# Kernel optimization log

Measured on AMD Instinct MI355X. Metric: run time of the kernel, lower is better.

## Reference

```python
import jax, jax.numpy as jnp
import numpy as np

N = 8192       # number of points
C = 16         # num_colors (size of color distribution)
DIM = 2        # spatial dim (GeometricLoss(dim=2))


def setup_inputs() -> dict:
    key = jax.random.key(0)
    k1, k2 = jax.random.split(key)
    outputs = jax.random.normal(k1, (N, C), dtype=jnp.float32)
    points = jax.random.normal(k2, (N, DIM), dtype=jnp.float32)
    return {"outputs": outputs, "points": points, "k": 5}


def reference(outputs, points, k):
    # cdist(points, points) via the squared-norm expansion (avoids [N,N,dim] tensor)
    sq = jnp.sum(points * points, axis=1)                      # [N]
    d2 = sq[:, None] + sq[None, :] - 2.0 * (points @ points.T)  # [N,N]
    dist = jnp.sqrt(jnp.maximum(d2, 0.0))
    # k+1 smallest distances per row; drop self (distance 0)
    _, idx = jax.lax.top_k(-dist, k + 1)                        # [N,k+1]
    idx = idx[:, 1:]                                            # [N,k]
    neighbor_outputs = outputs[idx]                             # [N,k,C] gather
    # ||out_i - out_j|| over color dim, mean over all (i, neighbor) pairs
    differences = jnp.linalg.norm(outputs[:, None, :] - neighbor_outputs, axis=2)
    return differences.mean()
```

## Files before the change

### kernel.cpp

```cpp
#include <hip/hip_runtime.h>


static constexpr int NPTS    = 8192;
static constexpr int KNN     = 5;
static constexpr int CH      = 16;
static constexpr int QPB     = 4;
static constexpr int THREADS = 256;
static constexpr int NBLK    = NPTS / QPB;
static constexpr int CAP     = 128;
static constexpr int NF4     = NPTS / 2;
static constexpr int ITERS   = NF4 / THREADS;
static constexpr int BAT     = 4;
static constexpr int NB      = ITERS / BAT;

__device__ __forceinline__ unsigned long long shfl_xor_u64(unsigned long long v, int m) {
    unsigned int lo = (unsigned int)v;
    unsigned int hi = (unsigned int)(v >> 32);
    lo = __shfl_xor(lo, m, 64);
    hi = __shfl_xor(hi, m, 64);
    return ((unsigned long long)hi << 32) | lo;
}

__global__ __launch_bounds__(256, 8) void knn_loss_kernel(
        const float* __restrict__ outputs,
        const float* __restrict__ points,
        float* __restrict__ partial) {
    const int tid  = threadIdx.x;
    const int wave = tid >> 6;
    const int lane = tid & 63;
    const int qbase = blockIdx.x * QPB;

    const float2* __restrict__ pts2 = (const float2*)points;
    const float4* __restrict__ pts4 = (const float4*)points;
    const float FINF = __int_as_float(0x7f800000);

    float pix[QPB], piy[QPB];
    #pragma unroll
    for (int q = 0; q < QPB; ++q) {
        const float2 p = pts2[qbase + q];
        pix[q] = p.x; piy[q] = p.y;
    }

    float acc[QPB];
    #pragma unroll
    for (int q = 0; q < QPB; ++q) acc[q] = FINF;

    for (int b = 0; b < NB; ++b) {
        float4 p[BAT];
        #pragma unroll
        for (int u = 0; u < BAT; ++u)
            p[u] = pts4[b * (BAT * THREADS) + u * THREADS + tid];
        #pragma unroll
        for (int u = 0; u < BAT; ++u) {
            #pragma unroll
            for (int q = 0; q < QPB; ++q) {
                const float dxa = pix[q] - p[u].x, dya = piy[q] - p[u].y;
                const float dxb = pix[q] - p[u].z, dyb = piy[q] - p[u].w;
                const float d2a = fmaf(dxa, dxa, dya * dya);
                const float d2b = fmaf(dxb, dxb, dyb * dyb);
                acc[q] = fminf(fminf(acc[q], d2a), d2b);
            }
        }
    }

    __shared__ float thrmin[QPB][THREADS];
    __shared__ unsigned long long buf[QPB][CAP];
    __shared__ int cnt[QPB];
    __shared__ float Ts[QPB];
    __shared__ float red[QPB];

    #pragma unroll
    for (int q = 0; q < QPB; ++q)
        thrmin[q][tid] = fmaxf(acc[q], 0.0f);
    if (tid < QPB) cnt[tid] = 0;
    __syncthreads();

    {
        const float4 tv = ((const float4*)thrmin[wave])[lane];
        float v = fminf(fminf(tv.x, tv.y), fminf(tv.z, tv.w));
        float T = 0.0f;
        #pragma unroll
        for (int t = 0; t < KNN + 1; ++t) {
            float m = v;
            #pragma unroll
            for (int d = 1; d < 64; d <<= 1) m = fminf(m, __shfl_xor(m, d, 64));
            if (v == m) v = FINF;
            T = m;
        }
        if (lane == 0) Ts[wave] = T;
    }
    __syncthreads();

    float Tq[QPB];
    #pragma unroll
    for (int q = 0; q < QPB; ++q) Tq[q] = Ts[q];

    for (int b = 0; b < NB; ++b) {
        float4 p[BAT];
        #pragma unroll
        for (int u = 0; u < BAT; ++u)
            p[u] = pts4[b * (BAT * THREADS) + u * THREADS + tid];
        #pragma unroll
        for (int u = 0; u < BAT; ++u) {
            const int it = b * (BAT * THREADS) + u * THREADS + tid;
            float g = FINF;
            #pragma unroll
            for (int q = 0; q < QPB; ++q) {
                const float dxa = pix[q] - p[u].x, dya = piy[q] - p[u].y;
                const float dxb = pix[q] - p[u].z, dyb = piy[q] - p[u].w;
                const float d2a = fmaf(dxa, dxa, dya * dya);
                const float d2b = fmaf(dxb, dxb, dyb * dyb);
                g = fminf(g, fminf(d2a, d2b) - Tq[q]);
            }
            if (g <= 0.0f) {
                #pragma unroll
                for (int q = 0; q < QPB; ++q) {
                    const float dxa = pix[q] - p[u].x, dya = piy[q] - p[u].y;
                    const float dxb = pix[q] - p[u].z, dyb = piy[q] - p[u].w;
                    const float d2a = fmaf(dxa, dxa, dya * dya);
                    const float d2b = fmaf(dxb, dxb, dyb * dyb);
                    if (d2a <= Tq[q]) {
                        const int pos = atomicAdd(&cnt[q], 1);
                        if (pos < CAP)
                            buf[q][pos] =
                                ((unsigned long long)__float_as_uint(fmaxf(d2a, 0.0f)) << 32)
                                | (unsigned int)(2 * it);
                    }
                    if (d2b <= Tq[q]) {
                        const int pos = atomicAdd(&cnt[q], 1);
                        if (pos < CAP)
                            buf[q][pos] =
                                ((unsigned long long)__float_as_uint(fmaxf(d2b, 0.0f)) << 32)
                                | (unsigned int)(2 * it + 1);
                    }
                }
            }
        }
    }
    __syncthreads();

    const unsigned long long INF64 = ~0ull;
    const int n = min(cnt[wave], CAP);
    unsigned long long a  = (lane      < n) ? buf[wave][lane]      : INF64;
    unsigned long long b2 = (lane + 64 < n) ? buf[wave][lane + 64] : INF64;
    if (b2 < a) { unsigned long long t = a; a = b2; b2 = t; }

    unsigned int myj = 0;
    int active = 0;
    #pragma unroll
    for (int t = 0; t < KNN + 1; ++t) {
        unsigned long long m = a;
        #pragma unroll
        for (int d = 1; d < 64; d <<= 1) {
            const unsigned long long x = shfl_xor_u64(m, d);
            if (x < m) m = x;
        }
        if (a == m) { a = b2; b2 = INF64; }
        if (t >= 1 && lane == t) { myj = (unsigned int)m; active = 1; }
    }

    float nrm = 0.0f;
    if (active) {
        const float4* oi = (const float4*)(outputs + (size_t)(qbase + wave) * CH);
        const float4* oj = (const float4*)(outputs + (size_t)myj * CH);
        float s = 0.0f;
        #pragma unroll
        for (int c = 0; c < 4; ++c) {
            const float4 x = oi[c], y = oj[c];
            const float dx = x.x - y.x, dy = x.y - y.y;
            const float dz = x.z - y.z, dw = x.w - y.w;
            s += dx * dx + dy * dy + dz * dz + dw * dw;
        }
        nrm = sqrtf(s);
    }
    #pragma unroll
    for (int d = 1; d < 64; d <<= 1) nrm += __shfl_xor(nrm, d, 64);

    if (lane == 0) red[wave] = nrm;
    __syncthreads();
    if (tid == 0)
        partial[blockIdx.x] = red[0] + red[1] + red[2] + red[3];
}

__global__ __launch_bounds__(256) void finalize_kernel(
        const float* __restrict__ partial, float* __restrict__ out) {
    double s = 0.0;
    for (int idx = threadIdx.x; idx < NBLK; idx += 256) s += (double)partial[idx];
    #pragma unroll
    for (int d = 1; d < 64; d <<= 1) s += __shfl_xor(s, d, 64);
    __shared__ double lds[4];
    const int wave = threadIdx.x >> 6;
    const int lane = threadIdx.x & 63;
    if (lane == 0) lds[wave] = s;
    __syncthreads();
    if (threadIdx.x == 0)
        out[0] = (float)((lds[0] + lds[1] + lds[2] + lds[3]) /
                         (double)((long long)NPTS * KNN));
}

extern "C" void kernel_launch(void* const* d_in, const int* in_sizes, int n_in,
                              void* d_out, int out_size, void* d_ws, size_t ws_size,
                              hipStream_t stream) {
    const float* outputs = (const float*)d_in[0];
    const float* points  = (const float*)d_in[1];
    float* partial = (float*)d_ws;
    float* out = (float*)d_out;

    knn_loss_kernel<<<NBLK, THREADS, 0, stream>>>(outputs, points, partial);
    finalize_kernel<<<1, 256, 0, stream>>>(partial, out);
}
```

Before: 84.82 us.

## Use 8 queries per 512-thread block with all points held in registers

Each block now handles 8 queries with 512 threads, one wave per query. Each thread loads its full share of points (8 float4) into registers once and reuses them for both the threshold pass and the candidate-collection pass instead of reloading per batch. Query coordinates and thresholds are made wave-uniform via readfirstlane. The per-point gate in the second pass now tests each query separately rather than a combined min across all queries. This raises register use and halves the block count, which may lower occupancy.

Measured after the change: 126.3 us. +48.9%, slower.

```diff
diff --git a/kernel.cpp b/kernel.cpp
--- a/kernel.cpp
+++ b/kernel.cpp
@@ -4,14 +4,12 @@
 static constexpr int NPTS    = 8192;
 static constexpr int KNN     = 5;
 static constexpr int CH      = 16;
-static constexpr int QPB     = 4;
-static constexpr int THREADS = 256;
+static constexpr int QPB     = 8;
+static constexpr int THREADS = 512;
 static constexpr int NBLK    = NPTS / QPB;
 static constexpr int CAP     = 128;
 static constexpr int NF4     = NPTS / 2;
 static constexpr int ITERS   = NF4 / THREADS;
-static constexpr int BAT     = 4;
-static constexpr int NB      = ITERS / BAT;
 
 __device__ __forceinline__ unsigned long long shfl_xor_u64(unsigned long long v, int m) {
     unsigned int lo = (unsigned int)v;
@@ -21,13 +19,17 @@
     return ((unsigned long long)hi << 32) | lo;
 }
 
-__global__ __launch_bounds__(256, 8) void knn_loss_kernel(
+__device__ __forceinline__ float rfl(float x) {
+    return __uint_as_float(__builtin_amdgcn_readfirstlane(__float_as_uint(x)));
+}
+
+__global__ __launch_bounds__(512, 8) void knn_loss_kernel(
         const float* __restrict__ outputs,
         const float* __restrict__ points,
         float* __restrict__ partial) {
-    const int tid  = threadIdx.x;
-    const int wave = tid >> 6;
-    const int lane = tid & 63;
+    const int tid   = threadIdx.x;
+    const int wave  = tid >> 6;
+    const int lane  = tid & 63;
     const int qbase = blockIdx.x * QPB;
 
     const float2* __restrict__ pts2 = (const float2*)points;
@@ -37,29 +39,27 @@
     float pix[QPB], piy[QPB];
     #pragma unroll
     for (int q = 0; q < QPB; ++q) {
-        const float2 p = pts2[qbase + q];
-        pix[q] = p.x; piy[q] = p.y;
-    }
+        const float2 pq = pts2[qbase + q];
+        pix[q] = rfl(pq.x); piy[q] = rfl(pq.y);
+    }
+
+    float4 p[ITERS];
+    #pragma unroll
+    for (int u = 0; u < ITERS; ++u)
+        p[u] = pts4[u * THREADS + tid];
 
     float acc[QPB];
     #pragma unroll
     for (int q = 0; q < QPB; ++q) acc[q] = FINF;
-
-    for (int b = 0; b < NB; ++b) {
-        float4 p[BAT];
-        #pragma unroll
-        for (int u = 0; u < BAT; ++u)
-            p[u] = pts4[b * (BAT * THREADS) + u * THREADS + tid];
-        #pragma unroll
-        for (int u = 0; u < BAT; ++u) {
-            #pragma unroll
-            for (int q = 0; q < QPB; ++q) {
-                const float dxa = pix[q] - p[u].x, dya = piy[q] - p[u].y;
-                const float dxb = pix[q] - p[u].z, dyb = piy[q] - p[u].w;
-                const float d2a = fmaf(dxa, dxa, dya * dya);
-                const float d2b = fmaf(dxb, dxb, dyb * dyb);
-                acc[q] = fminf(fminf(acc[q], d2a), d2b);
-            }
+    #pragma unroll
+    for (int u = 0; u < ITERS; ++u) {
+        #pragma unroll
+        for (int q = 0; q < QPB; ++q) {
+            const float dxa = pix[q] - p[u].x, dya = piy[q] - p[u].y;
+            const float dxb = pix[q] - p[u].z, dyb = piy[q] - p[u].w;
+            const float d2a = fmaf(dxa, dxa, dya * dya);
+            const float d2b = fmaf(dxb, dxb, dyb * dyb);
+            acc[q] = fminf(fminf(acc[q], d2a), d2b);
         }
     }
 
@@ -76,8 +76,10 @@
     __syncthreads();
 
     {
-        const float4 tv = ((const float4*)thrmin[wave])[lane];
-        float v = fminf(fminf(tv.x, tv.y), fminf(tv.z, tv.w));
+        float v = thrmin[wave][lane];
+        #pragma unroll
+        for (int r = 1; r < THREADS / 64; ++r)
+            v = fminf(v, thrmin[wave][lane + r * 64]);
         float T = 0.0f;
         #pragma unroll
         for (int t = 0; t < KNN + 1; ++t) {
@@ -93,46 +95,31 @@
 
     float Tq[QPB];
     #pragma unroll
-    for (int q = 0; q < QPB; ++q) Tq[q] = Ts[q];
-
-    for (int b = 0; b < NB; ++b) {
-        float4 p[BAT];
-        #pragma unroll
-        for (int u = 0; u < BAT; ++u)
-            p[u] = pts4[b * (BAT * THREADS) + u * THREADS + tid];
-        #pragma unroll
-        for (int u = 0; u < BAT; ++u) {
-            const int it = b * (BAT * THREADS) + u * THREADS + tid;
-            float g = FINF;
-            #pragma unroll
-            for (int q = 0; q < QPB; ++q) {
-                const float dxa = pix[q] - p[u].x, dya = piy[q] - p[u].y;
-                const float dxb = pix[q] - p[u].z, dyb = piy[q] - p[u].w;
-                const float d2a = fmaf(dxa, dxa, dya * dya);
-                const float d2b = fmaf(dxb, dxb, dyb * dyb);
-                g = fminf(g, fminf(d2a, d2b) - Tq[q]);
-            }
-            if (g <= 0.0f) {
-                #pragma unroll
-                for (int q = 0; q < QPB; ++q) {
-                    const float dxa = pix[q] - p[u].x, dya = piy[q] - p[u].y;
-                    const float dxb = pix[q] - p[u].z, dyb = piy[q] - p[u].w;
-                    const float d2a = fmaf(dxa, dxa, dya * dya);
-                    const float d2b = fmaf(dxb, dxb, dyb * dyb);
-                    if (d2a <= Tq[q]) {
-                        const int pos = atomicAdd(&cnt[q], 1);
-                        if (pos < CAP)
-                            buf[q][pos] =
-                                ((unsigned long long)__float_as_uint(fmaxf(d2a, 0.0f)) << 32)
-                                | (unsigned int)(2 * it);
-                    }
-                    if (d2b <= Tq[q]) {
-                        const int pos = atomicAdd(&cnt[q], 1);
-                        if (pos < CAP)
-                            buf[q][pos] =
-                                ((unsigned long long)__float_as_uint(fmaxf(d2b, 0.0f)) << 32)
-                                | (unsigned int)(2 * it + 1);
-                    }
+    for (int q = 0; q < QPB; ++q) Tq[q] = rfl(Ts[q]);
+
+    #pragma unroll
+    for (int u = 0; u < ITERS; ++u) {
+        const int jpair = u * THREADS + tid;
+        #pragma unroll
+        for (int q = 0; q < QPB; ++q) {
+            const float dxa = pix[q] - p[u].x, dya = piy[q] - p[u].y;
+            const float dxb = pix[q] - p[u].z, dyb = piy[q] - p[u].w;
+            const float d2a = fmaf(dxa, dxa, dya * dya);
+            const float d2b = fmaf(dxb, dxb, dyb * dyb);
+            if (fminf(d2a, d2b) <= Tq[q]) {
+                if (d2a <= Tq[q]) {
+                    const int pos = atomicAdd(&cnt[q], 1);
+                    if (pos < CAP)
+                        buf[q][pos] =
+                            ((unsigned long long)__float_as_uint(fmaxf(d2a, 0.0f)) << 32)
+                            | (unsigned int)(2 * jpair);
+                }
+                if (d2b <= Tq[q]) {
+                    const int pos = atomicAdd(&cnt[q], 1);
+                    if (pos < CAP)
+                        buf[q][pos] =
+                            ((unsigned long long)__float_as_uint(fmaxf(d2b, 0.0f)) << 32)
+                            | (unsigned int)(2 * jpair + 1);
                 }
             }
         }
@@ -178,8 +165,12 @@
 
     if (lane == 0) red[wave] = nrm;
     __syncthreads();
-    if (tid == 0)
-        partial[blockIdx.x] = red[0] + red[1] + red[2] + red[3];
+    if (tid == 0) {
+        float s = 0.0f;
+        #pragma unroll
+        for (int wv = 0; wv < QPB; ++wv) s += red[wv];
+        partial[blockIdx.x] = s;
+    }
 }
 
 __global__ __launch_bounds__(256) void finalize_kernel(
```
